# Kernel optimization log

Hardware: AMD Instinct MI355X
Metric: run time of the kernel (lower is better)

The kernel has to match this reference:

```python
import jax, jax.numpy as jnp
import numpy as np

DIM = 192; EXP = 2; QKB = 4
INNER = EXP * DIM          # 384
NH = INNER // QKB          # 96 heads
DH = QKB                   # 4 dims per head
Hs, Ws = 24, 24; S = Hs * Ws; B = 1; K = 3
EPS = 1e-6


def setup_inputs() -> dict:
    key = jax.random.key(0)
    ks = jax.random.split(key, 16)
    sm_up = (2.0 / (5.0 * DIM)) ** 0.5
    sm_dn = (2.0 / (5.0 * INNER)) ** 0.5
    def n(k, shape, s):
        return jax.random.normal(k, shape, jnp.float32) * s
    return {
        "x": jax.random.normal(ks[0], (B, S, DIM), jnp.float32),
        "d": jax.random.normal(ks[1], (B, S, DIM), jnp.float32),
        "ln_w": jnp.ones((DIM,), jnp.float32),
        "ln_b": jnp.zeros((DIM,), jnp.float32),
        "up_w": n(ks[2], (2 * INNER, DIM), sm_up),
        "up_b": jnp.zeros((2 * INNER,), jnp.float32),
        "dup_w": n(ks[3], (INNER, DIM), sm_up),
        "dup_b": jnp.zeros((INNER,), jnp.float32),
        "q_w": n(ks[4], (NH, DH, DH), sm_up), "q_b": jnp.zeros((INNER,), jnp.float32),
        "k_w": n(ks[5], (NH, DH, DH), sm_up), "k_b": jnp.zeros((INNER,), jnp.float32),
        "v_w": n(ks[6], (NH, DH, DH), sm_up), "v_b": jnp.zeros((INNER,), jnp.float32),
        "conv_w": n(ks[7], (INNER, K, K), 0.1), "conv_b": jnp.zeros((INNER,), jnp.float32),
        "ig_w": n(ks[8], (NH, 3 * INNER), 0.01),
        "ig_b": jax.random.normal(ks[9], (NH,), jnp.float32) * 0.1 - 3.0,
        "fg_w": jnp.zeros((NH, 3 * INNER), jnp.float32),
        "fg_b": jnp.linspace(3.0, 6.0, NH, dtype=jnp.float32),
        "onorm_w": jnp.ones((INNER,), jnp.float32),
        "skip": jnp.ones((INNER,), jnp.float32),
        "down_w": n(ks[10], (DIM, INNER), sm_dn),
        "down_b": jnp.zeros((DIM,), jnp.float32),
    }


def _headwise(x, w, b):
    # LinearHeadwiseExpand: block-diagonal linear, per-head DHxDH matrix
    Bx, Sx, _ = x.shape
    y = jnp.einsum('bsni,noi->bsno', x.reshape(Bx, Sx, NH, DH), w)
    return y.reshape(Bx, Sx, INNER) + b


def _mlstm(q, k, v, ig, fg, onorm_w):
    # parallel_stabilized_simple: q,k,v [B,NH,S,DH]; ig,fg [B,NH,S]
    Sq = q.shape[2]
    log_f = jax.nn.log_sigmoid(fg)                    # [B,NH,S]
    lfc = jnp.cumsum(log_f, axis=-1)                  # cumulative log forget
    logfm = lfc[..., :, None] - lfc[..., None, :]     # [B,NH,S,S]
    mask = jnp.tril(jnp.ones((Sq, Sq), dtype=bool))
    logD = jnp.where(mask, logfm + ig[..., None, :], -jnp.inf)
    maxD = jnp.max(logD, axis=-1, keepdims=True)      # [B,NH,S,1] stabilizer
    Dm = jnp.exp(logD - maxD)
    C = jnp.einsum('bnsd,bntd->bnst', q, k / (DH ** 0.5)) * Dm
    norm = jnp.maximum(jnp.abs(C.sum(-1, keepdims=True)), jnp.exp(-maxD))
    h = jnp.einsum('bnst,bntd->bnsd', C / (norm + EPS), v)
    # MultiHeadLayerNorm (group norm over DH per head, weight only)
    mu = h.mean(-1, keepdims=True)
    var = h.var(-1, keepdims=True)
    return (h - mu) / jnp.sqrt(var + 1e-5) * onorm_w.reshape(NH, DH)[None, :, None, :]


def _forward(x, d, ln_w, ln_b, up_w, up_b, dup_w, dup_b, q_w, q_b, k_w, k_b,
             v_w, v_b, conv_w, conv_b, ig_w, ig_b, fg_w, fg_b, onorm_w, skip,
             down_w, down_b):
    Bx, Sx, _ = x.shape
    # pre-norm LayerNorm
    mu = x.mean(-1, keepdims=True)
    var = x.var(-1, keepdims=True)
    xn = (x - mu) / jnp.sqrt(var + 1e-5) * ln_w + ln_b
    x_inner = xn @ up_w.T + up_b                      # [B,S,2*INNER]
    x_mlstm, z = jnp.split(x_inner, 2, axis=-1)
    d_mlstm = d @ dup_w.T + dup_b                     # dead code in original forward
    # depthwise 3x3 conv over the HxW token grid (SequenceConv2d, groups=INNER)
    kern = jnp.transpose(conv_w, (1, 2, 0))[:, :, None, :]   # HWIO
    xc = jax.lax.conv_general_dilated(
        x_mlstm.reshape(Bx, Hs, Ws, INNER), kern, (1, 1), 'SAME',
        dimension_numbers=('NHWC', 'HWIO', 'NHWC'),
        feature_group_count=INNER) + conv_b
    xa = jax.nn.silu(xc.reshape(Bx, Sx, INNER))
    q = _headwise(xa, q_w, q_b)
    k = _headwise(xa, k_w, k_b)
    v = _headwise(x_mlstm, v_w, v_b)
    gin = jnp.concatenate([q, k, v], axis=-1)         # [B,S,3*INNER]
    ig = (gin @ ig_w.T + ig_b).transpose(0, 2, 1)     # [B,NH,S]
    fg = (gin @ fg_w.T + fg_b).transpose(0, 2, 1)
    to_h = lambda t: t.reshape(Bx, Sx, NH, DH).transpose(0, 2, 1, 3)
    h = _mlstm(to_h(q), to_h(k), to_h(v), ig, fg, onorm_w)   # [B,NH,S,DH]
    h = h.transpose(0, 2, 1, 3).reshape(Bx, Sx, INNER)
    h = (h + skip * xa) * jax.nn.silu(z)
    return h @ down_w.T + down_b


def reference(x, d, ln_w, ln_b, up_w, up_b, dup_w, dup_b, q_w, q_b, k_w, k_b,
              v_w, v_b, conv_w, conv_b, ig_w, ig_b, fg_w, fg_b, onorm_w, skip,
              down_w, down_b):
    return _forward(x, d, ln_w, ln_b, up_w, up_b, dup_w, dup_b, q_w, q_b,
                    k_w, k_b, v_w, v_b, conv_w, conv_b, ig_w, ig_b, fg_w,
                    fg_b, onorm_w, skip, down_w, down_b)
```

## Files before the change

kernel.cpp:

```cpp
#include <hip/hip_runtime.h>
#include <math.h>

#define SEQ 576
#define DIM 192
#define INNER 384
#define NHEAD 96
#define HS 24
#define WSZ 24
#define GIN 1152
#define GKS 4

__global__ __launch_bounds__(256) void k_up(const float* __restrict__ x,
    const float* __restrict__ lnw, const float* __restrict__ lnb,
    const float* __restrict__ w, const float* __restrict__ b,
    float* __restrict__ out) {
  int m0 = blockIdx.x * 64, n0 = blockIdx.y * 32;
  __shared__ float As[DIM * 64];
  __shared__ float Bs[DIM * 32];
  __shared__ float mu[64], inv[64], ps[192];
  int t = threadIdx.x;
  for (int idx = t; idx < 64 * 48; idx += 256) {
    int r = idx / 48, k4 = idx % 48;
    float4 v = *(const float4*)&x[(m0 + r) * DIM + 4 * k4];
    int rw = r ^ (4 * (k4 & 15));
    As[(4 * k4 + 0) * 64 + rw] = v.x;
    As[(4 * k4 + 1) * 64 + rw] = v.y;
    As[(4 * k4 + 2) * 64 + rw] = v.z;
    As[(4 * k4 + 3) * 64 + rw] = v.w;
  }
  for (int idx = t; idx < 32 * 48; idx += 256) {
    int r = idx / 48, k4 = idx % 48;
    float4 v = *(const float4*)&w[(n0 + r) * DIM + 4 * k4];
    int rw = r ^ (4 * (k4 & 7));
    Bs[(4 * k4 + 0) * 32 + rw] = v.x;
    Bs[(4 * k4 + 1) * 32 + rw] = v.y;
    Bs[(4 * k4 + 2) * 32 + rw] = v.z;
    Bs[(4 * k4 + 3) * 32 + rw] = v.w;
  }
  __syncthreads();
  if (t < 192) {
    int r = t % 64, ph = t / 64;
    float s_ = 0.f;
    #pragma unroll 8
    for (int k = ph * 64; k < ph * 64 + 64; ++k)
      s_ += As[k * 64 + (r ^ (4 * ((k >> 2) & 15)))];
    ps[t] = s_;
  }
  __syncthreads();
  if (t < 64) mu[t] = (ps[t] + ps[64 + t] + ps[128 + t]) * (1.0f / DIM);
  __syncthreads();
  if (t < 192) {
    int r = t % 64, ph = t / 64;
    float m_ = mu[r], s_ = 0.f;
    #pragma unroll 8
    for (int k = ph * 64; k < ph * 64 + 64; ++k) {
      float d = As[k * 64 + (r ^ (4 * ((k >> 2) & 15)))] - m_;
      s_ += d * d;
    }
    ps[t] = s_;
  }
  __syncthreads();
  if (t < 64) inv[t] = rsqrtf((ps[t] + ps[64 + t] + ps[128 + t]) * (1.0f / DIM) + 1e-5f);
  __syncthreads();
  for (int idx = t; idx < 64 * DIM; idx += 256) {
    int k = idx >> 6, r0 = idx & 63;
    int m = r0 ^ (4 * ((k >> 2) & 15));
    As[idx] = (As[idx] - mu[m]) * inv[m] * lnw[k] + lnb[k];
  }
  __syncthreads();
  int gm = t >> 4, gn = t & 15;
  float acc[4][2];
  #pragma unroll
  for (int i = 0; i < 4; ++i)
    #pragma unroll
    for (int j = 0; j < 2; ++j) acc[i][j] = b[n0 + 2 * gn + j];
  #pragma unroll 4
  for (int kk = 0; kk < DIM; ++kk) {
    int mk = (kk >> 2) & 15, nk = 4 * ((kk >> 2) & 7);
    float4 a = *(const float4*)&As[kk * 64 + 4 * (gm ^ mk)];
    float2 bv = *(const float2*)&Bs[kk * 32 + ((2 * gn) ^ nk)];
    acc[0][0] += a.x * bv.x; acc[0][1] += a.x * bv.y;
    acc[1][0] += a.y * bv.x; acc[1][1] += a.y * bv.y;
    acc[2][0] += a.z * bv.x; acc[2][1] += a.z * bv.y;
    acc[3][0] += a.w * bv.x; acc[3][1] += a.w * bv.y;
  }
  #pragma unroll
  for (int i = 0; i < 4; ++i)
    *(float2*)&out[(m0 + 4 * gm + i) * (2 * INNER) + n0 + 2 * gn] =
        make_float2(acc[i][0], acc[i][1]);
}

__global__ __launch_bounds__(384) void k_cqkv(const float* __restrict__ xin,
    const float* __restrict__ cw, const float* __restrict__ cb,
    const float* __restrict__ qw, const float* __restrict__ qb,
    const float* __restrict__ kw, const float* __restrict__ kb,
    const float* __restrict__ vw, const float* __restrict__ vb,
    float* __restrict__ xa, float* __restrict__ ginT) {
  int s = blockIdx.x, t = threadIdx.x;
  int h = s / WSZ, wc = s % WSZ;
  __shared__ float xat[INNER], xmt[INNER];
  float acc = cb[t];
  #pragma unroll
  for (int kh = 0; kh < 3; ++kh) {
    int hh = h + kh - 1;
    if (hh < 0 || hh >= HS) continue;
    #pragma unroll
    for (int kw2 = 0; kw2 < 3; ++kw2) {
      int ww = wc + kw2 - 1;
      if (ww < 0 || ww >= WSZ) continue;
      acc += xin[(hh * WSZ + ww) * (2 * INNER) + t] * cw[t * 9 + kh * 3 + kw2];
    }
  }
  float sil = acc / (1.0f + __expf(-acc));
  xat[t] = sil;
  xa[s * INNER + t] = sil;
  xmt[t] = xin[s * (2 * INNER) + t];
  __syncthreads();
  int n = t >> 2, o = t & 3;
  const float* xah = xat + n * 4;
  const float* xmh = xmt + n * 4;
  float q = qb[t], k = kb[t], v = vb[t];
  #pragma unroll
  for (int i = 0; i < 4; ++i) {
    float xq = xah[i], xm = xmh[i];
    q += xq * qw[n * 16 + o * 4 + i];
    k += xq * kw[n * 16 + o * 4 + i];
    v += xm * vw[n * 16 + o * 4 + i];
  }
  ginT[t * SEQ + s]               = q;
  ginT[(INNER + t) * SEQ + s]     = k;
  ginT[(2 * INNER + t) * SEQ + s] = v;
}

#define GBK 288
__global__ __launch_bounds__(256) void k_gates(const float* __restrict__ ginT,
    const float* __restrict__ igw, const float* __restrict__ fgw,
    float* __restrict__ pig, float* __restrict__ pfg) {
  int bx = blockIdx.x, s0 = blockIdx.y * 64, ks = blockIdx.z;
  int k0 = ks * GBK;
  bool isig = bx < 3;
  int m0 = (isig ? bx : bx - 3) * 32;
  const float* wb = (isig ? igw : fgw) + m0 * GIN;
  __shared__ float Ws[GBK * 32];
  __shared__ float Gs[GBK * 64];
  int t = threadIdx.x;
  for (int idx = t; idx < 32 * 72; idx += 256) {
    int r = idx / 72, k4 = idx % 72;
    float4 v = *(const float4*)&wb[r * GIN + k0 + 4 * k4];
    int rw = r ^ (4 * (k4 & 7));
    Ws[(4 * k4 + 0) * 32 + rw] = v.x;
    Ws[(4 * k4 + 1) * 32 + rw] = v.y;
    Ws[(4 * k4 + 2) * 32 + rw] = v.z;
    Ws[(4 * k4 + 3) * 32 + rw] = v.w;
  }
  for (int idx = t; idx < GBK * 16; idx += 256) {
    int kk = idx / 16, s4 = idx % 16;
    *(float4*)&Gs[kk * 64 + 4 * s4] =
        *(const float4*)&ginT[(k0 + kk) * SEQ + s0 + 4 * s4];
  }
  __syncthreads();
  int gm = t >> 4, gn = t & 15;
  float acc[2][4] = {{0.f,0.f,0.f,0.f},{0.f,0.f,0.f,0.f}};
  #pragma unroll 4
  for (int kk = 0; kk < GBK; ++kk) {
    int nk = 4 * ((kk >> 2) & 7);
    float2 wv = *(const float2*)&Ws[kk * 32 + ((2 * gm) ^ nk)];
    float4 gv = *(const float4*)&Gs[kk * 64 + 4 * gn];
    acc[0][0] += wv.x * gv.x; acc[0][1] += wv.x * gv.y;
    acc[0][2] += wv.x * gv.z; acc[0][3] += wv.x * gv.w;
    acc[1][0] += wv.y * gv.x; acc[1][1] += wv.y * gv.y;
    acc[1][2] += wv.y * gv.z; acc[1][3] += wv.y * gv.w;
  }
  float* dstp = (isig ? pig : pfg) + ks * NHEAD * SEQ;
  #pragma unroll
  for (int i = 0; i < 2; ++i) {
    int mm = m0 + 2 * gm + i;
    *(float4*)&dstp[mm * SEQ + s0 + 4 * gn] =
        make_float4(acc[i][0], acc[i][1], acc[i][2], acc[i][3]);
  }
}

__global__ __launch_bounds__(576) void k_mlstm(const float* __restrict__ ginT,
    const float* __restrict__ pig, const float* __restrict__ pfg,
    const float* __restrict__ igb, const float* __restrict__ fgb,
    const float* __restrict__ onw, float* __restrict__ hout) {
  int n = blockIdx.x, hh = blockIdx.y, t = threadIdx.x;
  int base = 288 * hh;
  int cnt2 = base + 288;
  __shared__ float ksm[SEQ * 4], vsm[SEQ * 4], esm[SEQ];
  __shared__ float qsm[288 * 4];
  __shared__ float lfcs[SEQ], pms[SEQ];
  __shared__ float wsum[16], wmax[16];
  const int H4 = NHEAD * SEQ;
  int lane = t & 63, w = t >> 6;
  float ai = 0.f, lf = 0.f;
  if (t < cnt2) {
    float a0 = ginT[(INNER + n * 4 + 0) * SEQ + t] * 0.5f;
    float a1 = ginT[(INNER + n * 4 + 1) * SEQ + t] * 0.5f;
    float a2 = ginT[(INNER + n * 4 + 2) * SEQ + t] * 0.5f;
    float a3 = ginT[(INNER + n * 4 + 3) * SEQ + t] * 0.5f;
    *(float4*)&ksm[t * 4] = make_float4(a0, a1, a2, a3);
    float b0 = ginT[(2 * INNER + n * 4 + 0) * SEQ + t];
    float b1 = ginT[(2 * INNER + n * 4 + 1) * SEQ + t];
    float b2 = ginT[(2 * INNER + n * 4 + 2) * SEQ + t];
    float b3 = ginT[(2 * INNER + n * 4 + 3) * SEQ + t];
    *(float4*)&vsm[t * 4] = make_float4(b0, b1, b2, b3);
    if (t >= base) {
      int r = t - base;
      qsm[r * 4 + 0] = ginT[(n * 4 + 0) * SEQ + t];
      qsm[r * 4 + 1] = ginT[(n * 4 + 1) * SEQ + t];
      qsm[r * 4 + 2] = ginT[(n * 4 + 2) * SEQ + t];
      qsm[r * 4 + 3] = ginT[(n * 4 + 3) * SEQ + t];
    }
    int off = n * SEQ + t;
    ai = igb[n] + pig[off] + pig[off + H4] + pig[off + 2 * H4] + pig[off + 3 * H4];
    float af = fgb[n] + pfg[off] + pfg[off + H4] + pfg[off + 2 * H4] + pfg[off + 3 * H4];
    lf = (af >= 0.f) ? -log1pf(expf(-af)) : (af - log1pf(expf(af)));
  }
  float v = (t < cnt2) ? lf : 0.f;
  #pragma unroll
  for (int o2 = 1; o2 < 64; o2 <<= 1) {
    float u = __shfl_up(v, o2);
    if (lane >= o2) v += u;
  }
  if (lane == 63) wsum[w] = v;
  __syncthreads();
  if (t < 16) {
    float sv = (t < 9) ? wsum[t] : 0.f;
    #pragma unroll
    for (int o2 = 1; o2 < 16; o2 <<= 1) {
      float u = __shfl_up(sv, o2);
      if (t >= o2) sv += u;
    }
    wsum[t] = sv;
  }
  __syncthreads();
  float lfc = v + ((w > 0) ? wsum[w - 1] : 0.f);
  float e = ai - lfc;
  float m = (t < cnt2) ? e : -3.0e38f;
  #pragma unroll
  for (int o2 = 1; o2 < 64; o2 <<= 1) {
    float u = __shfl_up(m, o2);
    if (lane >= o2) m = fmaxf(m, u);
  }
  if (lane == 63) wmax[w] = m;
  __syncthreads();
  if (t < 16) {
    float sv = (t < 9) ? wmax[t] : -3.0e38f;
    #pragma unroll
    for (int o2 = 1; o2 < 16; o2 <<= 1) {
      float u = __shfl_up(sv, o2);
      if (t >= o2) sv = fmaxf(sv, u);
    }
    wmax[t] = sv;
  }
  __syncthreads();
  float pm = (w > 0) ? fmaxf(m, wmax[w - 1]) : m;
  if (t < cnt2) {
    esm[t] = e;
    lfcs[t] = lfc;
    pms[t] = pm;
  }
  __syncthreads();
  int rq = t >> 3, cq = t & 7;
  int s0 = base + 4 * rq;
  int N = s0 + 4;
  float pmv[4], qv[4][4];
  #pragma unroll
  for (int i = 0; i < 4; ++i) {
    pmv[i] = pms[s0 + i];
    *(float4*)&qv[i][0] = *(float4*)&qsm[(4 * rq + i) * 4];
  }
  int ch = (N + 7) >> 3;
  int lo = cq * ch, hi = min(lo + ch, N);
  float cs[4] = {0.f, 0.f, 0.f, 0.f};
  float hv[4][4];
  #pragma unroll
  for (int i = 0; i < 4; ++i)
    #pragma unroll
    for (int j = 0; j < 4; ++j) hv[i][j] = 0.f;
  for (int tt = lo; tt < hi; ++tt) {
    float e3 = esm[tt];
    float4 kv = *(const float4*)&ksm[tt * 4];
    float4 vv = *(const float4*)&vsm[tt * 4];
    #pragma unroll
    for (int i = 0; i < 4; ++i) {
      if (tt <= s0 + i) {
        float d = __expf(e3 - pmv[i]);
        float c = (qv[i][0] * kv.x + qv[i][1] * kv.y +
                   qv[i][2] * kv.z + qv[i][3] * kv.w) * d;
        cs[i] += c;
        hv[i][0] += c * vv.x; hv[i][1] += c * vv.y;
        hv[i][2] += c * vv.z; hv[i][3] += c * vv.w;
      }
    }
  }
  #pragma unroll
  for (int o2 = 4; o2 > 0; o2 >>= 1) {
    #pragma unroll
    for (int i = 0; i < 4; ++i) {
      cs[i] += __shfl_down(cs[i], o2);
      hv[i][0] += __shfl_down(hv[i][0], o2);
      hv[i][1] += __shfl_down(hv[i][1], o2);
      hv[i][2] += __shfl_down(hv[i][2], o2);
      hv[i][3] += __shfl_down(hv[i][3], o2);
    }
  }
  if (cq == 0) {
    #pragma unroll
    for (int i = 0; i < 4; ++i) {
      int s = s0 + i;
      float mxv = lfcs[s] + pmv[i];
      float norm = fmaxf(fabsf(cs[i]), __expf(-mxv)) + 1e-6f;
      float rr = 1.0f / norm;
      float h0 = hv[i][0] * rr, h1 = hv[i][1] * rr;
      float h2 = hv[i][2] * rr, h3 = hv[i][3] * rr;
      float mu = (h0 + h1 + h2 + h3) * 0.25f;
      float d0 = h0 - mu, d1 = h1 - mu, d2 = h2 - mu, d3 = h3 - mu;
      float var = (d0 * d0 + d1 * d1 + d2 * d2 + d3 * d3) * 0.25f;
      float inv = rsqrtf(var + 1e-5f);
      *(float4*)&hout[s * INNER + n * 4] = make_float4(
          d0 * inv * onw[n * 4 + 0], d1 * inv * onw[n * 4 + 1],
          d2 * inv * onw[n * 4 + 2], d3 * inv * onw[n * 4 + 3]);
    }
  }
}

#define KPA 388
__global__ __launch_bounds__(128) void k_down(const float* __restrict__ hmat,
    const float* __restrict__ xa, const float* __restrict__ xin,
    const float* __restrict__ skip, const float* __restrict__ dw,
    const float* __restrict__ db, float* __restrict__ out) {
  int m0 = blockIdx.x * 16, n0 = blockIdx.y * 32;
  __shared__ float As[16 * KPA];
  __shared__ float Bs[INNER * 32];
  int t = threadIdx.x;
  for (int idx = t; idx < 16 * 96; idx += 128) {
    int r = idx / 96, k4 = idx % 96;
    int s = m0 + r;
    float4 zv = *(const float4*)&xin[s * (2 * INNER) + INNER + 4 * k4];
    float4 hm = *(const float4*)&hmat[s * INNER + 4 * k4];
    float4 xv = *(const float4*)&xa[s * INNER + 4 * k4];
    float4 sk = *(const float4*)&skip[4 * k4];
    float z, sil;
    float4 o;
    z = zv.x; sil = z / (1.0f + __expf(-z)); o.x = (hm.x + sk.x * xv.x) * sil;
    z = zv.y; sil = z / (1.0f + __expf(-z)); o.y = (hm.y + sk.y * xv.y) * sil;
    z = zv.z; sil = z / (1.0f + __expf(-z)); o.z = (hm.z + sk.z * xv.z) * sil;
    z = zv.w; sil = z / (1.0f + __expf(-z)); o.w = (hm.w + sk.w * xv.w) * sil;
    *(float4*)&As[r * KPA + 4 * k4] = o;
  }
  for (int idx = t; idx < 32 * 96; idx += 128) {
    int r = idx / 96, k4 = idx % 96;
    float4 v = *(const float4*)&dw[(n0 + r) * INNER + 4 * k4];
    int rw = r ^ (4 * (k4 & 7));
    Bs[(4 * k4 + 0) * 32 + rw] = v.x;
    Bs[(4 * k4 + 1) * 32 + rw] = v.y;
    Bs[(4 * k4 + 2) * 32 + rw] = v.z;
    Bs[(4 * k4 + 3) * 32 + rw] = v.w;
  }
  __syncthreads();
  int gm = t >> 4, gn = t & 15;
  float acc[2][2];
  #pragma unroll
  for (int i = 0; i < 2; ++i)
    #pragma unroll
    for (int j = 0; j < 2; ++j) acc[i][j] = db[n0 + 2 * gn + j];
  #pragma unroll 4
  for (int kk = 0; kk < INNER; ++kk) {
    int nk = 4 * ((kk >> 2) & 7);
    float a0 = As[(2 * gm) * KPA + kk];
    float a1 = As[(2 * gm + 1) * KPA + kk];
    float2 bv = *(const float2*)&Bs[kk * 32 + ((2 * gn) ^ nk)];
    acc[0][0] += a0 * bv.x; acc[0][1] += a0 * bv.y;
    acc[1][0] += a1 * bv.x; acc[1][1] += a1 * bv.y;
  }
  #pragma unroll
  for (int i = 0; i < 2; ++i)
    *(float2*)&out[(m0 + 2 * gm + i) * DIM + n0 + 2 * gn] =
        make_float2(acc[i][0], acc[i][1]);
}

extern "C" void kernel_launch(void* const* d_in, const int* in_sizes, int n_in,
                              void* d_out, int out_size, void* d_ws, size_t ws_size,
                              hipStream_t stream) {
  const float* x      = (const float*)d_in[0];
  const float* ln_w   = (const float*)d_in[2];
  const float* ln_b   = (const float*)d_in[3];
  const float* up_w   = (const float*)d_in[4];
  const float* up_b   = (const float*)d_in[5];
  const float* q_w    = (const float*)d_in[8];
  const float* q_b    = (const float*)d_in[9];
  const float* k_w    = (const float*)d_in[10];
  const float* k_b    = (const float*)d_in[11];
  const float* v_w    = (const float*)d_in[12];
  const float* v_b    = (const float*)d_in[13];
  const float* conv_w = (const float*)d_in[14];
  const float* conv_b = (const float*)d_in[15];
  const float* ig_w   = (const float*)d_in[16];
  const float* ig_b   = (const float*)d_in[17];
  const float* fg_w   = (const float*)d_in[18];
  const float* fg_b   = (const float*)d_in[19];
  const float* onorm_w= (const float*)d_in[20];
  const float* skip   = (const float*)d_in[21];
  const float* down_w = (const float*)d_in[22];
  const float* down_b = (const float*)d_in[23];
  float* out = (float*)d_out;

  float* ws     = (float*)d_ws;
  float* xinner = ws;
  float* xa     = xinner + SEQ * 2 * INNER;
  float* ginT   = xa + SEQ * INNER;
  float* pig    = ginT + GIN * SEQ;
  float* pfg    = pig + GKS * NHEAD * SEQ;
  float* hbuf   = pfg + GKS * NHEAD * SEQ;

  k_up   <<<dim3(9, 24), 256, 0, stream>>>(x, ln_w, ln_b, up_w, up_b, xinner);
  k_cqkv <<<SEQ, 384, 0, stream>>>(xinner, conv_w, conv_b,
                                   q_w, q_b, k_w, k_b, v_w, v_b, xa, ginT);
  k_gates<<<dim3(6, 9, GKS), 256, 0, stream>>>(ginT, ig_w, fg_w, pig, pfg);
  k_mlstm<<<dim3(NHEAD, 2), 576, 0, stream>>>(ginT, pig, pfg, ig_b, fg_b, onorm_w, hbuf);
  k_down <<<dim3(36, 6), 128, 0, stream>>>(hbuf, xa, xinner, skip, down_w, down_b, out);
}
```

Measured before the change: 101.5 us.

## Fold headwise q/k/v weights into gate weights and recompute qkv in mLSTM

Measured after the change: 92.60 us (median of 2 runs). -8.8%, faster.

```diff
diff --git a/kernel.cpp b/kernel.cpp
--- a/kernel.cpp
+++ b/kernel.cpp
@@ -7,7 +7,6 @@
 #define NHEAD 96
 #define HS 24
 #define WSZ 24
-#define GIN 1152
 #define GKS 4
 
 __global__ __launch_bounds__(256) void k_up(const float* __restrict__ x,
@@ -92,13 +91,13 @@
 
 __global__ __launch_bounds__(384) void k_cqkv(const float* __restrict__ xin,
     const float* __restrict__ cw, const float* __restrict__ cb,
-    const float* __restrict__ qw, const float* __restrict__ qb,
-    const float* __restrict__ kw, const float* __restrict__ kb,
-    const float* __restrict__ vw, const float* __restrict__ vb,
-    float* __restrict__ xa, float* __restrict__ ginT) {
+    const float* __restrict__ igw, const float* __restrict__ fgw,
+    const float* __restrict__ qw, const float* __restrict__ kw,
+    const float* __restrict__ vw,
+    float* __restrict__ xa, float* __restrict__ xaT,
+    float* __restrict__ xmT, float* __restrict__ weff) {
   int s = blockIdx.x, t = threadIdx.x;
   int h = s / WSZ, wc = s % WSZ;
-  __shared__ float xat[INNER], xmt[INNER];
   float acc = cb[t];
   #pragma unroll
   for (int kh = 0; kh < 3; ++kh) {
@@ -112,41 +111,44 @@
     }
   }
   float sil = acc / (1.0f + __expf(-acc));
-  xat[t] = sil;
   xa[s * INNER + t] = sil;
-  xmt[t] = xin[s * (2 * INNER) + t];
-  __syncthreads();
-  int n = t >> 2, o = t & 3;
-  const float* xah = xat + n * 4;
-  const float* xmh = xmt + n * 4;
-  float q = qb[t], k = kb[t], v = vb[t];
-  #pragma unroll
-  for (int i = 0; i < 4; ++i) {
-    float xq = xah[i], xm = xmh[i];
-    q += xq * qw[n * 16 + o * 4 + i];
-    k += xq * kw[n * 16 + o * 4 + i];
-    v += xm * vw[n * 16 + o * 4 + i];
-  }
-  ginT[t * SEQ + s]               = q;
-  ginT[(INNER + t) * SEQ + s]     = k;
-  ginT[(2 * INNER + t) * SEQ + s] = v;
-}
-
-#define GBK 288
-__global__ __launch_bounds__(256) void k_gates(const float* __restrict__ ginT,
-    const float* __restrict__ igw, const float* __restrict__ fgw,
+  xaT[t * SEQ + s] = sil;
+  xmT[t * SEQ + s] = xin[s * (2 * INNER) + t];
+  if (s < 192) {
+    const float* wg = (s < NHEAD) ? (igw + s * 1152) : (fgw + (s - NHEAD) * 1152);
+    for (int cp = t; cp < 768; cp += 384) {
+      float wv = 0.f;
+      if (cp < 384) {
+        int n = cp >> 2, j = cp & 3;
+        #pragma unroll
+        for (int o = 0; o < 4; ++o)
+          wv += wg[4 * n + o] * qw[n * 16 + o * 4 + j]
+              + wg[384 + 4 * n + o] * kw[n * 16 + o * 4 + j];
+      } else {
+        int c2 = cp - 384;
+        int n = c2 >> 2, j = c2 & 3;
+        #pragma unroll
+        for (int o = 0; o < 4; ++o)
+          wv += wg[768 + 4 * n + o] * vw[n * 16 + o * 4 + j];
+      }
+      weff[s * 768 + cp] = wv;
+    }
+  }
+}
+
+#define GBK 192
+__global__ __launch_bounds__(256) void k_gates(const float* __restrict__ gT,
+    const float* __restrict__ weff,
     float* __restrict__ pig, float* __restrict__ pfg) {
-  int bx = blockIdx.x, s0 = blockIdx.y * 64, ks = blockIdx.z;
-  int k0 = ks * GBK;
-  bool isig = bx < 3;
-  int m0 = (isig ? bx : bx - 3) * 32;
-  const float* wb = (isig ? igw : fgw) + m0 * GIN;
+  int m0 = blockIdx.x * 32, s0 = blockIdx.y * 64, ksl = blockIdx.z;
+  int k0 = ksl * GBK;
+  const float* wb = weff + m0 * 768;
   __shared__ float Ws[GBK * 32];
   __shared__ float Gs[GBK * 64];
   int t = threadIdx.x;
-  for (int idx = t; idx < 32 * 72; idx += 256) {
-    int r = idx / 72, k4 = idx % 72;
-    float4 v = *(const float4*)&wb[r * GIN + k0 + 4 * k4];
+  for (int idx = t; idx < 32 * 48; idx += 256) {
+    int r = idx / 48, k4 = idx % 48;
+    float4 v = *(const float4*)&wb[r * 768 + k0 + 4 * k4];
     int rw = r ^ (4 * (k4 & 7));
     Ws[(4 * k4 + 0) * 32 + rw] = v.x;
     Ws[(4 * k4 + 1) * 32 + rw] = v.y;
@@ -156,7 +158,7 @@
   for (int idx = t; idx < GBK * 16; idx += 256) {
     int kk = idx / 16, s4 = idx % 16;
     *(float4*)&Gs[kk * 64 + 4 * s4] =
-        *(const float4*)&ginT[(k0 + kk) * SEQ + s0 + 4 * s4];
+        *(const float4*)&gT[(k0 + kk) * SEQ + s0 + 4 * s4];
   }
   __syncthreads();
   int gm = t >> 4, gn = t & 15;
@@ -171,18 +173,25 @@
     acc[1][0] += wv.y * gv.x; acc[1][1] += wv.y * gv.y;
     acc[1][2] += wv.y * gv.z; acc[1][3] += wv.y * gv.w;
   }
-  float* dstp = (isig ? pig : pfg) + ks * NHEAD * SEQ;
   #pragma unroll
   for (int i = 0; i < 2; ++i) {
     int mm = m0 + 2 * gm + i;
-    *(float4*)&dstp[mm * SEQ + s0 + 4 * gn] =
+    float* dst = (mm < NHEAD) ? (pig + ksl * NHEAD * SEQ + mm * SEQ)
+                              : (pfg + ksl * NHEAD * SEQ + (mm - NHEAD) * SEQ);
+    *(float4*)&dst[s0 + 4 * gn] =
         make_float4(acc[i][0], acc[i][1], acc[i][2], acc[i][3]);
   }
 }
 
-__global__ __launch_bounds__(576) void k_mlstm(const float* __restrict__ ginT,
+__global__ __launch_bounds__(576) void k_mlstm(const float* __restrict__ xaT,
+    const float* __restrict__ xmT,
     const float* __restrict__ pig, const float* __restrict__ pfg,
+    const float* __restrict__ igw, const float* __restrict__ fgw,
     const float* __restrict__ igb, const float* __restrict__ fgb,
+    const float* __restrict__ qw, const float* __restrict__ kw,
+    const float* __restrict__ vw,
+    const float* __restrict__ qb, const float* __restrict__ kb,
+    const float* __restrict__ vb,
     const float* __restrict__ onw, float* __restrict__ hout) {
   int n = blockIdx.x, hh = blockIdx.y, t = threadIdx.x;
   int base = 288 * hh;
@@ -190,31 +199,55 @@
   __shared__ float ksm[SEQ * 4], vsm[SEQ * 4], esm[SEQ];
   __shared__ float qsm[288 * 4];
   __shared__ float lfcs[SEQ], pms[SEQ];
-  __shared__ float wsum[16], wmax[16];
+  __shared__ float wsum[16], wmax[16], bdi[16], bdf[16];
   const int H4 = NHEAD * SEQ;
   int lane = t & 63, w = t >> 6;
+  {
+    float b1 = (t < 384) ? qb[t] : kb[t - 384];
+    float b2 = (t < 192) ? kb[192 + t] : vb[t - 192];
+    float w1 = igw[n * 1152 + t], w2 = igw[n * 1152 + 576 + t];
+    float f1 = fgw[n * 1152 + t], f2 = fgw[n * 1152 + 576 + t];
+    float pi = w1 * b1 + w2 * b2;
+    float pf = f1 * b1 + f2 * b2;
+    #pragma unroll
+    for (int o2 = 32; o2 > 0; o2 >>= 1) {
+      pi += __shfl_down(pi, o2);
+      pf += __shfl_down(pf, o2);
+    }
+    if (lane == 0) { bdi[w] = pi; bdf[w] = pf; }
+  }
+  float psi = 0.f, psf = 0.f;
+  if (t < cnt2) {
+    const float* xan = xaT + 4 * n * SEQ;
+    float a0 = xan[t], a1 = xan[SEQ + t], a2 = xan[2 * SEQ + t], a3 = xan[3 * SEQ + t];
+    const float* xmn = xmT + 4 * n * SEQ;
+    float m0_ = xmn[t], m1_ = xmn[SEQ + t], m2_ = xmn[2 * SEQ + t], m3_ = xmn[3 * SEQ + t];
+    #pragma unroll
+    for (int o = 0; o < 4; ++o) {
+      float kv = kb[4 * n + o] + kw[n * 16 + o * 4 + 0] * a0 + kw[n * 16 + o * 4 + 1] * a1
+               + kw[n * 16 + o * 4 + 2] * a2 + kw[n * 16 + o * 4 + 3] * a3;
+      ksm[t * 4 + o] = kv * 0.5f;
+      vsm[t * 4 + o] = vb[4 * n + o] + vw[n * 16 + o * 4 + 0] * m0_ + vw[n * 16 + o * 4 + 1] * m1_
+               + vw[n * 16 + o * 4 + 2] * m2_ + vw[n * 16 + o * 4 + 3] * m3_;
+    }
+    if (t >= base) {
+      int r = t - base;
+      #pragma unroll
+      for (int o = 0; o < 4; ++o)
+        qsm[r * 4 + o] = qb[4 * n + o] + qw[n * 16 + o * 4 + 0] * a0 + qw[n * 16 + o * 4 + 1] * a1
+                 + qw[n * 16 + o * 4 + 2] * a2 + qw[n * 16 + o * 4 + 3] * a3;
+    }
+    int off = n * SEQ + t;
+    psi = pig[off] + pig[off + H4] + pig[off + 2 * H4] + pig[off + 3 * H4];
+    psf = pfg[off] + pfg[off + H4] + pfg[off + 2 * H4] + pfg[off + 3 * H4];
+  }
+  __syncthreads();
+  float bdI = bdi[0] + bdi[1] + bdi[2] + bdi[3] + bdi[4] + bdi[5] + bdi[6] + bdi[7] + bdi[8];
+  float bdF = bdf[0] + bdf[1] + bdf[2] + bdf[3] + bdf[4] + bdf[5] + bdf[6] + bdf[7] + bdf[8];
   float ai = 0.f, lf = 0.f;
   if (t < cnt2) {
-    float a0 = ginT[(INNER + n * 4 + 0) * SEQ + t] * 0.5f;
-    float a1 = ginT[(INNER + n * 4 + 1) * SEQ + t] * 0.5f;
-    float a2 = ginT[(INNER + n * 4 + 2) * SEQ + t] * 0.5f;
-    float a3 = ginT[(INNER + n * 4 + 3) * SEQ + t] * 0.5f;
-    *(float4*)&ksm[t * 4] = make_float4(a0, a1, a2, a3);
-    float b0 = ginT[(2 * INNER + n * 4 + 0) * SEQ + t];
-    float b1 = ginT[(2 * INNER + n * 4 + 1) * SEQ + t];
-    float b2 = ginT[(2 * INNER + n * 4 + 2) * SEQ + t];
-    float b3 = ginT[(2 * INNER + n * 4 + 3) * SEQ + t];
-    *(float4*)&vsm[t * 4] = make_float4(b0, b1, b2, b3);
-    if (t >= base) {
-      int r = t - base;
-      qsm[r * 4 + 0] = ginT[(n * 4 + 0) * SEQ + t];
-      qsm[r * 4 + 1] = ginT[(n * 4 + 1) * SEQ + t];
-      qsm[r * 4 + 2] = ginT[(n * 4 + 2) * SEQ + t];
-      qsm[r * 4 + 3] = ginT[(n * 4 + 3) * SEQ + t];
-    }
-    int off = n * SEQ + t;
-    ai = igb[n] + pig[off] + pig[off + H4] + pig[off + 2 * H4] + pig[off + 3 * H4];
-    float af = fgb[n] + pfg[off] + pfg[off + H4] + pfg[off + 2 * H4] + pfg[off + 3 * H4];
+    ai = igb[n] + bdI + psi;
+    float af = fgb[n] + bdF + psf;
     lf = (af >= 0.f) ? -log1pf(expf(-af)) : (af - log1pf(expf(af)));
   }
   float v = (t < cnt2) ? lf : 0.f;
@@ -410,15 +443,19 @@
   float* ws     = (float*)d_ws;
   float* xinner = ws;
   float* xa     = xinner + SEQ * 2 * INNER;
-  float* ginT   = xa + SEQ * INNER;
-  float* pig    = ginT + GIN * SEQ;
+  float* xaT    = xa + SEQ * INNER;
+  float* xmT    = xaT + INNER * SEQ;
+  float* weff   = xmT + INNER * SEQ;
+  float* pig    = weff + 192 * 768;
   float* pfg    = pig + GKS * NHEAD * SEQ;
   float* hbuf   = pfg + GKS * NHEAD * SEQ;
 
   k_up   <<<dim3(9, 24), 256, 0, stream>>>(x, ln_w, ln_b, up_w, up_b, xinner);
-  k_cqkv <<<SEQ, 384, 0, stream>>>(xinner, conv_w, conv_b,
-                                   q_w, q_b, k_w, k_b, v_w, v_b, xa, ginT);
-  k_gates<<<dim3(6, 9, GKS), 256, 0, stream>>>(ginT, ig_w, fg_w, pig, pfg);
-  k_mlstm<<<dim3(NHEAD, 2), 576, 0, stream>>>(ginT, pig, pfg, ig_b, fg_b, onorm_w, hbuf);
+  k_cqkv <<<SEQ, 384, 0, stream>>>(xinner, conv_w, conv_b, ig_w, fg_w,
+                                   q_w, k_w, v_w, xa, xaT, xmT, weff);
+  k_gates<<<dim3(6, 9, GKS), 256, 0, stream>>>(xaT, weff, pig, pfg);
+  k_mlstm<<<dim3(NHEAD, 2), 576, 0, stream>>>(xaT, xmT, pig, pfg, ig_w, fg_w,
+                                              ig_b, fg_b, q_w, k_w, v_w,
+                                              q_b, k_b, v_b, onorm_w, hbuf);
   k_down <<<dim3(36, 6), 128, 0, stream>>>(hbuf, xa, xinner, skip, down_w, down_b, out);
 }
```
